# Performance work log

Measured on AMD Instinct MI355X. Metric: run time of the kernel, lower is better.

Reference implementation:

```python
import jax, jax.numpy as jnp
import numpy as np

ALPHA = 0.0005
TAU = 0.2


def setup_inputs() -> dict:
    key = jax.random.key(0)
    k1, k2, k3 = jax.random.split(key, 3)
    output = jax.random.normal(k1, (8192, 1000), dtype=jnp.float32)
    target = jax.random.normal(k2, (8192, 1000), dtype=jnp.float32)
    conv_w = jax.random.normal(k3, (256, 256, 128, 3), dtype=jnp.float32)
    return {"output": output, "target": target, "conv_w": conv_w}


def reference(output, target, conv_w):
    # base loss (nn.MSELoss with default 'mean' reduction)
    loss = jnp.mean((output - target) ** 2)

    # Diversity regularizer: pairwise cosine similarity between slices
    # conv_w[:, :, i, :] along dim 2 ('filters' = size(2) in the original).
    F = conv_w.shape[2]
    # V: [F, D] with D = out_ch * in_ch * kw
    V = jnp.transpose(conv_w, (2, 0, 1, 3)).reshape(F, -1)
    norms = jnp.linalg.norm(V, axis=1)                      # [F]
    G = (V @ V.T) / (norms[:, None] * norms[None, :])       # [F, F] cosine Gram

    # keep entries with tau < sim <= 1 and i != j
    offdiag = ~jnp.eye(F, dtype=bool)
    mask = (G > TAU) & (G <= 1.0) & offdiag
    reg = jnp.sum(jnp.where(mask, G, jnp.zeros((), dtype=G.dtype)))

    return loss + ALPHA * reg
```

## Files before the change

### kernel.cpp

```cpp
#include <hip/hip_runtime.h>
#include <hip/hip_bf16.h>


typedef __attribute__((ext_vector_type(8))) short bf16x8;
typedef __attribute__((ext_vector_type(4))) float f32x4;

#define ALPHA 0.0005f
#define TAU 0.2f

#define FDIM 128
#define NBLK 256
#define GRAM_ELEMS 16384
#define NPAIRQ 8192
#define MSE_N4 2048000
#define NTILES 256

__device__ __forceinline__ unsigned int pack_bf2(float lo, float hi) {
    union { float f; unsigned int u; } a, b;
    a.f = lo; b.f = hi;
    unsigned int al = (a.u + 0x7fffu + ((a.u >> 16) & 1u)) >> 16;
    unsigned int bh = (b.u + 0x7fffu + ((b.u >> 16) & 1u)) & 0xffff0000u;
    return (al & 0xffffu) | bh;
}

__device__ __forceinline__ bf16x8 make_frag(const float3& a, const float3& b) {
    union { bf16x8 v; unsigned int u[4]; } r;
    r.u[0] = pack_bf2(a.x, a.y);
    r.u[1] = pack_bf2(a.z, b.x);
    r.u[2] = pack_bf2(b.y, b.z);
    r.u[3] = 0;
    return r.v;
}

__device__ __forceinline__ void load_oct(const float* __restrict__ lp,
                                         float3 (&L)[8][2]) {
#pragma unroll
    for (int tt = 0; tt < 8; ++tt)
#pragma unroll
        for (int e = 0; e < 2; ++e)
            L[tt][e] = *reinterpret_cast<const float3*>(lp + tt * 48 + e * 384);
    __builtin_amdgcn_sched_barrier(0);
}

__device__ __forceinline__ void step_oct(const float3 (&L)[8][2],
                                         f32x4 (&acc)[8][8]) {
    bf16x8 fr[8];
#pragma unroll
    for (int tt = 0; tt < 8; ++tt) fr[tt] = make_frag(L[tt][0], L[tt][1]);
#pragma unroll
    for (int r = 0; r < 8; ++r)
#pragma unroll
        for (int c = 0; c < 8; ++c)
            acc[r][c] = __builtin_amdgcn_mfma_f32_16x16x32_bf16(
                fr[r], fr[c], acc[r][c], 0, 0, 0);
}

__global__ void __launch_bounds__(256, 1) fused_kernel(
        const float* __restrict__ o, const float* __restrict__ t,
        const float* __restrict__ conv,
        float* __restrict__ mse_part, unsigned int* __restrict__ pp) {
    __shared__ unsigned int pk[4][NPAIRQ];
    __shared__ float red[4];
    const int tid = threadIdx.x;
    const int lane = tid & 63;
    const int wave = tid >> 6;
    const int g = lane >> 4;
    const int fl = lane & 15;

    const int W = blockIdx.x * 4 + wave;
    const float* lp = conv + (size_t)W * 24576 + (2 * g) * 384 + fl * 3;

    float3 L0[8][2], L1[8][2];
    load_oct(lp, L0);

    {
        const int gid = blockIdx.x * 256 + tid;
        const f32x4* o4 = reinterpret_cast<const f32x4*>(o);
        const f32x4* t4 = reinterpret_cast<const f32x4*>(t);
        float s = 0.f;
#pragma unroll 8
        for (int p = 0; p < 31; ++p) {
            const int i = gid + p * 65536;
            f32x4 a = o4[i], b = t4[i];
            f32x4 d = a - b;
            s += d[0]*d[0] + d[1]*d[1] + d[2]*d[2] + d[3]*d[3];
        }
        if (gid < MSE_N4 - 31 * 65536) {
            const int i = gid + 31 * 65536;
            f32x4 a = o4[i], b = t4[i];
            f32x4 d = a - b;
            s += d[0]*d[0] + d[1]*d[1] + d[2]*d[2] + d[3]*d[3];
        }
        for (int off = 32; off; off >>= 1) s += __shfl_down(s, off);
        if (lane == 0) red[wave] = s;
        __syncthreads();
        if (tid == 0) mse_part[blockIdx.x] = red[0] + red[1] + red[2] + red[3];
    }

    f32x4 acc[8][8];
#pragma unroll
    for (int r = 0; r < 8; ++r)
#pragma unroll
        for (int c = 0; c < 8; ++c) acc[r][c] = (f32x4)0.f;

#pragma unroll
    for (int oo = 0; oo < 8; oo += 2) {
        load_oct(lp + (oo + 1) * 3072, L1);
        step_oct(L0, acc);
        if (oo + 2 < 8) load_oct(lp + (oo + 2) * 3072, L0);
        step_oct(L1, acc);
    }

#pragma unroll
    for (int m = 0; m < 4; ++m)
#pragma unroll
        for (int c = 0; c < 8; ++c)
#pragma unroll
            for (int j = 0; j < 4; ++j)
                pk[wave][(m * 16 + g * 4 + j) * FDIM + c * 16 + fl] =
                    pack_bf2(acc[2 * m][c][j], acc[2 * m + 1][c][j]);
    __syncthreads();

    unsigned int* myp = pp + (size_t)blockIdx.x * NPAIRQ;
    for (int e = tid; e < NPAIRQ; e += 256) {
        float lo = 0.f, hi = 0.f;
#pragma unroll
        for (int w = 0; w < 4; ++w) {
            const unsigned int v = pk[w][e];
            lo += __uint_as_float(v << 16);
            hi += __uint_as_float(v & 0xffff0000u);
        }
        myp[e] = pack_bf2(lo, hi);
    }
}

__global__ void __launch_bounds__(256) reduce_kernel(
        const unsigned int* __restrict__ pp, float* __restrict__ gram) {
    __shared__ float red[16][16][2];
    const int tid = threadIdx.x;
    const int u = tid & 15;
    const int s = tid >> 4;
    const int qq = blockIdx.x * 16 + u;
    float lo = 0.f, hi = 0.f;
#pragma unroll 8
    for (int b = s * 16; b < s * 16 + 16; ++b) {
        const unsigned int v = pp[(size_t)b * NPAIRQ + qq];
        lo += __uint_as_float(v << 16);
        hi += __uint_as_float(v & 0xffff0000u);
    }
    red[s][u][0] = lo; red[s][u][1] = hi;
    __syncthreads();
    if (tid < 32) {
        const int u2 = tid >> 1, h = tid & 1;
        float x = 0.f;
#pragma unroll
        for (int s2 = 0; s2 < 16; ++s2) x += red[s2][u2][h];
        gram[(blockIdx.x * 16 + u2) * 2 + h] = x;
    }
}

__global__ void __launch_bounds__(256) finalize_kernel(
        const float* __restrict__ gram, const float* __restrict__ mse_part,
        float* __restrict__ out) {
    __shared__ float rn[FDIM];
    __shared__ float redS[4], redM[4];
    const int tid = threadIdx.x;
    if (tid < FDIM) {
        const int row = tid;
        const int pr = (row >> 5) * 16 + (row & 15);
        const int h = (row >> 4) & 1;
        rn[row] = rsqrtf(gram[(pr * FDIM + row) * 2 + h]);
    }
    __syncthreads();
    float s = 0.f;
    for (int i = tid; i < GRAM_ELEMS; i += 256) {
        const int h = i & 1;
        const int qq = i >> 1;
        const int col = qq & 127;
        const int pr = qq >> 7;
        const int row = (pr >> 4) * 32 + (pr & 15) + (h << 4);
        const float g = gram[i] * rn[row] * rn[col];
        if (row != col && g > TAU && g <= 1.0f) s += g;
    }
    float m = mse_part[tid];
    for (int off = 32; off; off >>= 1) {
        s += __shfl_down(s, off);
        m += __shfl_down(m, off);
    }
    if ((tid & 63) == 0) { redS[tid >> 6] = s; redM[tid >> 6] = m; }
    __syncthreads();
    if (tid == 0)
        out[0] = (redM[0] + redM[1] + redM[2] + redM[3]) * (1.0f / 8192000.0f) +
                 ALPHA * (redS[0] + redS[1] + redS[2] + redS[3]);
}

extern "C" void kernel_launch(void* const* d_in, const int* in_sizes, int n_in,
                              void* d_out, int out_size, void* d_ws, size_t ws_size,
                              hipStream_t stream) {
    const float* output = (const float*)d_in[0];
    const float* target = (const float*)d_in[1];
    const float* conv   = (const float*)d_in[2];
    float* out = (float*)d_out;

    float* wsf       = (float*)d_ws;
    float* mse_part  = wsf;
    float* gram      = wsf + 256;
    unsigned int* pp = (unsigned int*)(wsf + 256 + GRAM_ELEMS);
    (void)ws_size;

    fused_kernel<<<NBLK, 256, 0, stream>>>(output, target, conv, mse_part, pp);
    reduce_kernel<<<NPAIRQ / 16, 256, 0, stream>>>(pp, gram);
    finalize_kernel<<<1, 256, 0, stream>>>(gram, mse_part, out);
}
```

Baseline: 57.94 us.

## Split Gram and MSE work into separate blocks and tile Gram rows across waves

```diff
diff --git a/kernel.cpp b/kernel.cpp
--- a/kernel.cpp
+++ b/kernel.cpp
@@ -9,11 +9,11 @@
 #define TAU 0.2f
 
 #define FDIM 128
-#define NBLK 256
+#define NGRAM 1024
+#define NMSE 2048
+#define NPAIRQ 8192
 #define GRAM_ELEMS 16384
-#define NPAIRQ 8192
 #define MSE_N4 2048000
-#define NTILES 256
 
 __device__ __forceinline__ unsigned int pack_bf2(float lo, float hi) {
     union { float f; unsigned int u; } a, b;
@@ -32,61 +32,53 @@
     return r.v;
 }
 
+struct OctB { float3 B[8][2]; float3 A[2][2]; };
+
 __device__ __forceinline__ void load_oct(const float* __restrict__ lp,
-                                         float3 (&L)[8][2]) {
-#pragma unroll
-    for (int tt = 0; tt < 8; ++tt)
-#pragma unroll
-        for (int e = 0; e < 2; ++e)
-            L[tt][e] = *reinterpret_cast<const float3*>(lp + tt * 48 + e * 384);
+                                         const float* __restrict__ lpA,
+                                         OctB& o) {
+#pragma unroll
+    for (int tt = 0; tt < 8; ++tt) {
+        o.B[tt][0] = *reinterpret_cast<const float3*>(lp + tt * 48);
+        o.B[tt][1] = *reinterpret_cast<const float3*>(lp + tt * 48 + 384);
+    }
+#pragma unroll
+    for (int a = 0; a < 2; ++a) {
+        o.A[a][0] = *reinterpret_cast<const float3*>(lpA + a * 48);
+        o.A[a][1] = *reinterpret_cast<const float3*>(lpA + a * 48 + 384);
+    }
     __builtin_amdgcn_sched_barrier(0);
 }
 
-__device__ __forceinline__ void step_oct(const float3 (&L)[8][2],
-                                         f32x4 (&acc)[8][8]) {
-    bf16x8 fr[8];
-#pragma unroll
-    for (int tt = 0; tt < 8; ++tt) fr[tt] = make_frag(L[tt][0], L[tt][1]);
-#pragma unroll
-    for (int r = 0; r < 8; ++r)
-#pragma unroll
-        for (int c = 0; c < 8; ++c)
-            acc[r][c] = __builtin_amdgcn_mfma_f32_16x16x32_bf16(
-                fr[r], fr[c], acc[r][c], 0, 0, 0);
-}
-
-__global__ void __launch_bounds__(256, 1) fused_kernel(
+__device__ __forceinline__ void consume_oct(const OctB& o,
+                                            f32x4 (&acc0)[8], f32x4 (&acc1)[8]) {
+    const bf16x8 fA0 = make_frag(o.A[0][0], o.A[0][1]);
+    const bf16x8 fA1 = make_frag(o.A[1][0], o.A[1][1]);
+#pragma unroll
+    for (int cc = 0; cc < 8; ++cc) {
+        const bf16x8 fb = make_frag(o.B[cc][0], o.B[cc][1]);
+        acc0[cc] = __builtin_amdgcn_mfma_f32_16x16x32_bf16(fA0, fb, acc0[cc], 0, 0, 0);
+        acc1[cc] = __builtin_amdgcn_mfma_f32_16x16x32_bf16(fA1, fb, acc1[cc], 0, 0, 0);
+    }
+}
+
+__global__ void __launch_bounds__(256, 2) fused_kernel(
         const float* __restrict__ o, const float* __restrict__ t,
         const float* __restrict__ conv,
         float* __restrict__ mse_part, unsigned int* __restrict__ pp) {
-    __shared__ unsigned int pk[4][NPAIRQ];
     __shared__ float red[4];
     const int tid = threadIdx.x;
     const int lane = tid & 63;
     const int wave = tid >> 6;
-    const int g = lane >> 4;
-    const int fl = lane & 15;
-
-    const int W = blockIdx.x * 4 + wave;
-    const float* lp = conv + (size_t)W * 24576 + (2 * g) * 384 + fl * 3;
-
-    float3 L0[8][2], L1[8][2];
-    load_oct(lp, L0);
-
-    {
-        const int gid = blockIdx.x * 256 + tid;
+
+    if (blockIdx.x >= NGRAM) {
+        const int mb = blockIdx.x - NGRAM;
+        const int gid = mb * 256 + tid;
         const f32x4* o4 = reinterpret_cast<const f32x4*>(o);
         const f32x4* t4 = reinterpret_cast<const f32x4*>(t);
         float s = 0.f;
-#pragma unroll 8
-        for (int p = 0; p < 31; ++p) {
-            const int i = gid + p * 65536;
-            f32x4 a = o4[i], b = t4[i];
-            f32x4 d = a - b;
-            s += d[0]*d[0] + d[1]*d[1] + d[2]*d[2] + d[3]*d[3];
-        }
-        if (gid < MSE_N4 - 31 * 65536) {
-            const int i = gid + 31 * 65536;
+#pragma unroll 4
+        for (int i = gid; i < MSE_N4; i += NMSE * 256) {
             f32x4 a = o4[i], b = t4[i];
             f32x4 d = a - b;
             s += d[0]*d[0] + d[1]*d[1] + d[2]*d[2] + d[3]*d[3];
@@ -94,43 +86,41 @@
         for (int off = 32; off; off >>= 1) s += __shfl_down(s, off);
         if (lane == 0) red[wave] = s;
         __syncthreads();
-        if (tid == 0) mse_part[blockIdx.x] = red[0] + red[1] + red[2] + red[3];
-    }
-
-    f32x4 acc[8][8];
-#pragma unroll
-    for (int r = 0; r < 8; ++r)
-#pragma unroll
-        for (int c = 0; c < 8; ++c) acc[r][c] = (f32x4)0.f;
+        if (tid == 0) mse_part[mb] = red[0] + red[1] + red[2] + red[3];
+        return;
+    }
+
+    const int g = lane >> 4;
+    const int fl = lane & 15;
+    const float* lp  = conv + (size_t)blockIdx.x * 24576 + (2 * g) * 384 + fl * 3;
+    const float* lpA = lp + wave * 96;
+
+    f32x4 acc0[8], acc1[8];
+#pragma unroll
+    for (int cc = 0; cc < 8; ++cc) { acc0[cc] = (f32x4)0.f; acc1[cc] = (f32x4)0.f; }
+
+    OctB O0, O1;
+    load_oct(lp,        lpA,        O0);
+    load_oct(lp + 3072, lpA + 3072, O1);
 
 #pragma unroll
     for (int oo = 0; oo < 8; oo += 2) {
-        load_oct(lp + (oo + 1) * 3072, L1);
-        step_oct(L0, acc);
-        if (oo + 2 < 8) load_oct(lp + (oo + 2) * 3072, L0);
-        step_oct(L1, acc);
-    }
-
-#pragma unroll
-    for (int m = 0; m < 4; ++m)
-#pragma unroll
-        for (int c = 0; c < 8; ++c)
-#pragma unroll
-            for (int j = 0; j < 4; ++j)
-                pk[wave][(m * 16 + g * 4 + j) * FDIM + c * 16 + fl] =
-                    pack_bf2(acc[2 * m][c][j], acc[2 * m + 1][c][j]);
-    __syncthreads();
+        consume_oct(O0, acc0, acc1);
+        if (oo + 2 < 8) load_oct(lp + (oo + 2) * 3072, lpA + (oo + 2) * 3072, O0);
+        consume_oct(O1, acc0, acc1);
+        if (oo + 3 < 8) load_oct(lp + (oo + 3) * 3072, lpA + (oo + 3) * 3072, O1);
+    }
 
     unsigned int* myp = pp + (size_t)blockIdx.x * NPAIRQ;
-    for (int e = tid; e < NPAIRQ; e += 256) {
-        float lo = 0.f, hi = 0.f;
-#pragma unroll
-        for (int w = 0; w < 4; ++w) {
-            const unsigned int v = pk[w][e];
-            lo += __uint_as_float(v << 16);
-            hi += __uint_as_float(v & 0xffff0000u);
+    const int rsub = (lane >> 4) << 2;
+#pragma unroll
+    for (int cc = 0; cc < 8; ++cc) {
+        const int col = cc * 16 + fl;
+#pragma unroll
+        for (int j = 0; j < 4; ++j) {
+            const int pr = wave * 16 + rsub + j;
+            myp[pr * FDIM + col] = pack_bf2(acc0[cc][j], acc1[cc][j]);
         }
-        myp[e] = pack_bf2(lo, hi);
     }
 }
 
@@ -143,7 +133,7 @@
     const int qq = blockIdx.x * 16 + u;
     float lo = 0.f, hi = 0.f;
 #pragma unroll 8
-    for (int b = s * 16; b < s * 16 + 16; ++b) {
+    for (int b = s * 64; b < s * 64 + 64; ++b) {
         const unsigned int v = pp[(size_t)b * NPAIRQ + qq];
         lo += __uint_as_float(v << 16);
         hi += __uint_as_float(v & 0xffff0000u);
@@ -179,10 +169,12 @@
         const int col = qq & 127;
         const int pr = qq >> 7;
         const int row = (pr >> 4) * 32 + (pr & 15) + (h << 4);
-        const float g = gram[i] * rn[row] * rn[col];
-        if (row != col && g > TAU && g <= 1.0f) s += g;
-    }
-    float m = mse_part[tid];
+        const float gv = gram[i] * rn[row] * rn[col];
+        if (row != col && gv > TAU && gv <= 1.0f) s += gv;
+    }
+    float m = 0.f;
+#pragma unroll 8
+    for (int j = 0; j < 8; ++j) m += mse_part[tid * 8 + j];
     for (int off = 32; off; off >>= 1) {
         s += __shfl_down(s, off);
         m += __shfl_down(m, off);
@@ -204,11 +196,12 @@
 
     float* wsf       = (float*)d_ws;
     float* mse_part  = wsf;
-    float* gram      = wsf + 256;
-    unsigned int* pp = (unsigned int*)(wsf + 256 + GRAM_ELEMS);
+    float* gram      = wsf + NMSE;
+    unsigned int* pp = (unsigned int*)(wsf + NMSE + GRAM_ELEMS);
     (void)ws_size;
 
-    fused_kernel<<<NBLK, 256, 0, stream>>>(output, target, conv, mse_part, pp);
+    fused_kernel<<<NGRAM + NMSE, 256, 0, stream>>>(output, target, conv,
+                                                   mse_part, pp);
     reduce_kernel<<<NPAIRQ / 16, 256, 0, stream>>>(pp, gram);
     finalize_kernel<<<1, 256, 0, stream>>>(gram, mse_part, out);
 }
```

Result: slower. 71.96 us (+24.2%).
